# Kernel optimization log

Hardware: AMD Instinct MI355X
Metric: run time of the kernel (lower is better)

Reference implementation:

```python
import jax, jax.numpy as jnp
import numpy as np

B, N, E = 128, 2000, 2000
EMBED, HIDDEN = 256, 512


def setup_inputs() -> dict:
    key = jax.random.key(0)
    k1, k2, k3, k4, k5, k6, k7 = jax.random.split(key, 7)
    node_embeddings = jax.random.normal(k1, (B, N, EMBED), dtype=jnp.float32)
    locs = jax.random.uniform(k2, (B, N, 2), dtype=jnp.float32)
    edge_list = jax.random.randint(k3, (B, E, 2), 0, N, dtype=jnp.int64)
    in_dim = 2 * EMBED + 1
    # Kaiming-ish init for the two Linear layers of edge_scorer
    W1 = jax.random.normal(k4, (in_dim, HIDDEN), dtype=jnp.float32) / np.sqrt(in_dim)
    b1 = jnp.zeros((HIDDEN,), dtype=jnp.float32)
    W2 = jax.random.normal(k5, (HIDDEN, 1), dtype=jnp.float32) / np.sqrt(HIDDEN)
    b2 = jnp.zeros((1,), dtype=jnp.float32)
    return {
        "node_embeddings": node_embeddings,
        "locs": locs,
        "edge_list": edge_list,
        "delete_bias": 0,
        "W1": W1,
        "b1": b1,
        "W2": W2,
        "b2": b2,
    }


def reference(node_embeddings, locs, edge_list, delete_bias, W1, b1, W2, b2):
    # valid mask for -1-padded edges
    valid = (edge_list[..., 0] >= 0) & (edge_list[..., 1] >= 0)  # (B, E)
    edges = jnp.clip(edge_list, 0, None)
    bidx = jnp.arange(node_embeddings.shape[0])[:, None]  # (B, 1)
    i, j = edges[..., 0], edges[..., 1]  # (B, E)
    emb_i = node_embeddings[bidx, i]  # (B, E, D)
    emb_j = node_embeddings[bidx, j]  # (B, E, D)
    d = locs[bidx, i] - locs[bidx, j]  # (B, E, 2)
    dist = jnp.sqrt(jnp.sum(d * d, axis=-1, keepdims=True))  # (B, E, 1)
    feats = jnp.concatenate([emb_i, emb_j, dist], axis=-1)  # (B, E, 2D+1)
    h = jax.nn.relu(jnp.einsum('bef,fh->beh', feats, W1) + b1)
    logits = (jnp.einsum('beh,ho->beo', h, W2) + b2)[..., 0]  # (B, E)
    logits = jnp.where(valid, logits, -jnp.inf)
    return logits + jnp.float32(delete_bias)
```

## Files before the change

kernel.cpp:

```cpp
#include <hip/hip_runtime.h>
#include <math.h>

#define EMBED    256
#define HIDDEN   512
#define Nn       2000
#define Ee       2000
#define BM       128
#define TILES    8
#define NBLK     250
#define NTHREADS 512
#define FP       264

typedef __attribute__((ext_vector_type(8)))  short bf16x8;
typedef __attribute__((ext_vector_type(16))) float f32x16;

static __device__ __forceinline__ short f2bf(float f) {
  unsigned u = __builtin_bit_cast(unsigned, f);
  u += 0x7fffu + ((u >> 16) & 1u);
  return (short)(u >> 16);
}

static __device__ __forceinline__ bf16x8 cvt8(float4 a, float4 b) {
  bf16x8 v;
  v[0]=f2bf(a.x); v[1]=f2bf(a.y); v[2]=f2bf(a.z); v[3]=f2bf(a.w);
  v[4]=f2bf(b.x); v[5]=f2bf(b.y); v[6]=f2bf(b.z); v[7]=f2bf(b.w);
  return v;
}

#define LBAR() do { asm volatile("s_waitcnt lgkmcnt(0)" ::: "memory"); \
                    __builtin_amdgcn_s_barrier(); \
                    asm volatile("" ::: "memory"); } while (0)

__global__ void w1f_kernel(const float* __restrict__ W1, short* __restrict__ W1F) {
  const int t  = blockIdx.x * 512 + threadIdx.x;
  const int l  = t & 63;
  const int tk = (t >> 6) & 31;
  const int tn = t >> 11;
  const int n  = tn * 32 + (l & 31);
  const int k0 = tk * 16 + (l >> 5) * 8;
  bf16x8 v;
#pragma unroll
  for (int q = 0; q < 8; ++q)
    v[q] = f2bf(W1[(size_t)(k0 + q) * HIDDEN + n]);
  *(bf16x8*)(W1F + (size_t)t * 8) = v;
}

__global__ __launch_bounds__(NTHREADS, 2)
void edge_kernel(const float* __restrict__ emb, const float* __restrict__ locs,
                 const int* __restrict__ edges, const int* __restrict__ dbias,
                 const float* __restrict__ W1, const float* __restrict__ b1,
                 const float* __restrict__ W2, const float* __restrict__ b2,
                 const short* __restrict__ W1F, float* __restrict__ out)
{
  __shared__ short feat[2][BM][FP];
  __shared__ float b1_s[HIDDEN], w513_s[HIDDEN], w2_s[HIDDEN];
  __shared__ float part_s[8][BM];
  __shared__ float dist_s[2][BM];
  __shared__ int   valid_s[2][BM];
  __shared__ int   ibase_s[2][BM], jbase_s[2][BM];

  const int tid = threadIdx.x;

  const int orig = blockIdx.x;
  const int xcd  = orig & 7;
  const int idx  = orig >> 3;
  const int sbid = (xcd < 2 ? xcd * 32 : 64 + (xcd - 2) * 31) + idx;
  const int eblk = sbid * (TILES * BM);

  b1_s[tid]   = b1[tid];
  w513_s[tid] = W1[(size_t)512 * HIDDEN + tid];
  w2_s[tid]   = W2[tid];
  const float b2s_base = b2[0] + (float)dbias[0];

  auto do_meta = [&](int T) {
    const int g  = eblk + T * BM + tid;
    const int b  = g / Ee;
    const int i0 = edges[2 * g];
    const int j0 = edges[2 * g + 1];
    valid_s[T & 1][tid] = (i0 >= 0) && (j0 >= 0);
    const int ib = b * Nn + (i0 < 0 ? 0 : i0);
    const int jb = b * Nn + (j0 < 0 ? 0 : j0);
    ibase_s[T & 1][tid] = ib;
    jbase_s[T & 1][tid] = jb;
    const float dx = locs[2 * (size_t)ib]     - locs[2 * (size_t)jb];
    const float dy = locs[2 * (size_t)ib + 1] - locs[2 * (size_t)jb + 1];
    dist_s[T & 1][tid] = sqrtf(dx * dx + dy * dy);
  };

  if (tid < BM) do_meta(0);
  LBAR();

  const int sq = tid & 7;
  const int eh = tid >> 3;
  const int lane = tid & 63;
  const int w    = tid >> 6;
  const int ln31 = lane & 31;
  const int kg   = lane >> 5;

#pragma unroll
  for (int r = 0; r < 2; ++r) {
    const int el = r * 64 + eh;
    const float* src = emb + (size_t)ibase_s[0][el] * EMBED + sq * 8;
#pragma unroll
    for (int m = 0; m < 4; ++m) {
      float4 a  = *(const float4*)(src + m * 64);
      float4 b4 = *(const float4*)(src + m * 64 + 4);
      *(bf16x8*)&feat[0][el][(sq + 8 * m) * 8] = cvt8(a, b4);
    }
  }
  LBAR();

  f32x16 acc[4][2];
#pragma unroll
  for (int et = 0; et < 4; ++et)
#pragma unroll
    for (int nt = 0; nt < 2; ++nt)
#pragma unroll
      for (int q = 0; q < 16; ++q) acc[et][nt][q] = 0.f;

  const short* wfb = W1F + (size_t)(w * 2 * 32) * 512 + lane * 8;

#pragma unroll 1
  for (int p = 0; p < 2 * TILES; ++p) {
    const int bb   = p & 1;
    const int nbuf = bb ^ 1;
    const int half = p & 1;
    const int tps  = (p + 1) >> 1;
    const int sh   = (p + 1) & 1;
    const bool stg = p < 2 * TILES - 1;

    bf16x8 wc0 = *(const bf16x8*)(wfb + (size_t)(half * 16) * 512);
    bf16x8 wc1 = *(const bf16x8*)(wfb + (size_t)(32 + half * 16) * 512);

    float4 hg00, hg01, hg10, hg11;

#pragma unroll
    for (int ks = 0; ks < 16; ++ks) {
      bf16x8 wn0, wn1;
      if (ks < 15) {
        wn0 = *(const bf16x8*)(wfb + (size_t)(half * 16 + ks + 1) * 512);
        wn1 = *(const bf16x8*)(wfb + (size_t)(32 + half * 16 + ks + 1) * 512);
      }

      if (stg && (ks & 3) == 0) {
        const int g2 = ks >> 2;
        const int el = (g2 >> 1) * 64 + eh;
        const int rb = sh ? jbase_s[tps & 1][el] : ibase_s[tps & 1][el];
        const float* src = emb + (size_t)rb * EMBED + sq * 8 + (g2 & 1) * 128;
        hg00 = *(const float4*)(src);
        hg01 = *(const float4*)(src + 4);
        hg10 = *(const float4*)(src + 64);
        hg11 = *(const float4*)(src + 68);
      }
      if (stg && (ks & 3) == 3) {
        const int g2 = ks >> 2;
        const int el = (g2 >> 1) * 64 + eh;
        const int mb = (g2 & 1) * 2;
        *(bf16x8*)&feat[nbuf][el][(sq + 8 * mb) * 8]       = cvt8(hg00, hg01);
        *(bf16x8*)&feat[nbuf][el][(sq + 8 * (mb + 1)) * 8] = cvt8(hg10, hg11);
      }
      if ((p & 1) == 0 && ks == 1 && tid < BM && (p >> 1) + 1 < TILES)
        do_meta((p >> 1) + 1);

#pragma unroll
      for (int et = 0; et < 4; ++et) {
        bf16x8 fb = *(const bf16x8*)(&feat[bb][et * 32 + ln31][ks * 16 + kg * 8]);
        acc[et][0] = __builtin_amdgcn_mfma_f32_32x32x16_bf16(wc0, fb, acc[et][0], 0, 0, 0);
        acc[et][1] = __builtin_amdgcn_mfma_f32_32x32x16_bf16(wc1, fb, acc[et][1], 0, 0, 0);
      }
      wc0 = wn0; wc1 = wn1;
    }
    LBAR();

    if (p & 1) {
      const int t   = p >> 1;
      const int mb2 = t & 1;
      float dv[4], ps[4];
#pragma unroll
      for (int et = 0; et < 4; ++et) {
        dv[et] = dist_s[mb2][et * 32 + ln31];
        ps[et] = 0.f;
      }
#pragma unroll
      for (int nt = 0; nt < 2; ++nt) {
#pragma unroll
        for (int r = 0; r < 16; ++r) {
          const int n = w * 64 + nt * 32 + (r & 3) + ((r >> 2) << 3) + (kg << 2);
          const float bias = b1_s[n];
          const float wd   = w513_s[n];
          const float w2v  = w2_s[n];
#pragma unroll
          for (int et = 0; et < 4; ++et) {
            float pv = acc[et][nt][r] + bias + dv[et] * wd;
            ps[et] += fmaxf(pv, 0.f) * w2v;
          }
        }
      }
#pragma unroll
      for (int et = 0; et < 4; ++et) ps[et] += __shfl_xor(ps[et], 32, 64);
      if (lane < 32) {
#pragma unroll
        for (int et = 0; et < 4; ++et) part_s[w][et * 32 + ln31] = ps[et];
      }
      LBAR();
      if (tid < BM) {
        float s = 0.f;
#pragma unroll
        for (int wv = 0; wv < 8; ++wv) s += part_s[wv][tid];
        float logit = s + b2s_base;
        if (!valid_s[mb2][tid]) logit = -__builtin_inff();
        out[eblk + t * BM + tid] = logit;
      }
#pragma unroll
      for (int et = 0; et < 4; ++et)
#pragma unroll
        for (int nt = 0; nt < 2; ++nt)
#pragma unroll
          for (int q = 0; q < 16; ++q) acc[et][nt][q] = 0.f;
    }
  }
}

extern "C" void kernel_launch(void* const* d_in, const int* in_sizes, int n_in,
                              void* d_out, int out_size, void* d_ws, size_t ws_size,
                              hipStream_t stream) {
  const float* emb   = (const float*)d_in[0];
  const float* locs  = (const float*)d_in[1];
  const int*   edges = (const int*)d_in[2];
  const int*   dbias = (const int*)d_in[3];
  const float* W1    = (const float*)d_in[4];
  const float* b1    = (const float*)d_in[5];
  const float* W2    = (const float*)d_in[6];
  const float* b2    = (const float*)d_in[7];
  float*       out   = (float*)d_out;
  short*       W1F   = (short*)d_ws;

  w1f_kernel<<<dim3(64), dim3(512), 0, stream>>>(W1, W1F);
  edge_kernel<<<dim3(NBLK), dim3(NTHREADS), 0, stream>>>(
      emb, locs, edges, dbias, W1, b1, W2, b2, (const short*)W1F, out);
}
```

Baseline: 151.7 us.

## Split K loop into 64-wide phases with triple-buffered LDS and deeper gather prefetch

Restructures the main loop from 16 half-tile phases of K=256 into 64 phases of K=64. The feature staging buffer becomes three small 72-wide buffers, and each embedding gather is issued two phases before it is consumed. All eight W1 fragments for a phase are loaded up front, and the MFMA cluster runs at raised wave priority with sched_barriers fencing the stages. The intent is to hide global gather latency behind more compute and shrink LDS use. In exchange it adds a block barrier per phase, four times as many as before, and more register pressure from the extra weight and prefetch buffers.

```diff
diff --git a/kernel.cpp b/kernel.cpp
--- a/kernel.cpp
+++ b/kernel.cpp
@@ -9,7 +9,9 @@
 #define TILES    8
 #define NBLK     250
 #define NTHREADS 512
-#define FP       264
+#define PHT      8
+#define NPH      (TILES * PHT)
+#define FP       72
 
 typedef __attribute__((ext_vector_type(8)))  short bf16x8;
 typedef __attribute__((ext_vector_type(16))) float f32x16;
@@ -52,7 +54,7 @@
                  const float* __restrict__ W2, const float* __restrict__ b2,
                  const short* __restrict__ W1F, float* __restrict__ out)
 {
-  __shared__ short feat[2][BM][FP];
+  __shared__ short feat[3][BM][FP];
   __shared__ float b1_s[HIDDEN], w513_s[HIDDEN], w2_s[HIDDEN];
   __shared__ float part_s[8][BM];
   __shared__ float dist_s[2][BM];
@@ -71,6 +73,14 @@
   w513_s[tid] = W1[(size_t)512 * HIDDEN + tid];
   w2_s[tid]   = W2[tid];
   const float b2s_base = b2[0] + (float)dbias[0];
+
+  const int lane = tid & 63;
+  const int w    = tid >> 6;
+  const int ln31 = lane & 31;
+  const int kg   = lane >> 5;
+
+  const int e  = tid >> 2;
+  const int sq = tid & 3;
 
   auto do_meta = [&](int T) {
     const int g  = eblk + T * BM + tid;
@@ -87,98 +97,93 @@
     dist_s[T & 1][tid] = sqrtf(dx * dx + dy * dy);
   };
 
+  auto issue_g = [&](int pp, float4* g) {
+    const int T    = pp >> 3;
+    const int ph   = pp & 7;
+    const int side = ph >> 2;
+    const int q    = ph & 3;
+    const int rb = side ? jbase_s[T & 1][e] : ibase_s[T & 1][e];
+    const float* src = emb + (size_t)rb * EMBED + q * 64 + sq * 16;
+    g[0] = *(const float4*)(src);
+    g[1] = *(const float4*)(src + 4);
+    g[2] = *(const float4*)(src + 8);
+    g[3] = *(const float4*)(src + 12);
+  };
+  auto land_g = [&](int pp, const float4* g) {
+    const int buf = pp % 3;
+    *(bf16x8*)&feat[buf][e][sq * 16]     = cvt8(g[0], g[1]);
+    *(bf16x8*)&feat[buf][e][sq * 16 + 8] = cvt8(g[2], g[3]);
+  };
+
   if (tid < BM) do_meta(0);
   LBAR();
-
-  const int sq = tid & 7;
-  const int eh = tid >> 3;
-  const int lane = tid & 63;
-  const int w    = tid >> 6;
-  const int ln31 = lane & 31;
-  const int kg   = lane >> 5;
-
-#pragma unroll
-  for (int r = 0; r < 2; ++r) {
-    const int el = r * 64 + eh;
-    const float* src = emb + (size_t)ibase_s[0][el] * EMBED + sq * 8;
-#pragma unroll
-    for (int m = 0; m < 4; ++m) {
-      float4 a  = *(const float4*)(src + m * 64);
-      float4 b4 = *(const float4*)(src + m * 64 + 4);
-      *(bf16x8*)&feat[0][el][(sq + 8 * m) * 8] = cvt8(a, b4);
+  float4 ga[4], gb4[4];
+  issue_g(0, ga);
+  issue_g(1, gb4);
+  land_g(0, ga);
+  land_g(1, gb4);
+  issue_g(2, ga);
+  LBAR();
+
+  f32x16 acc[4][2];
+#pragma unroll
+  for (int et = 0; et < 4; ++et)
+#pragma unroll
+    for (int nt = 0; nt < 2; ++nt)
+#pragma unroll
+      for (int q = 0; q < 16; ++q) acc[et][nt][q] = 0.f;
+
+  const short* wfb = W1F + (size_t)(w * 2 * 32) * 512 + lane * 8;
+
+#pragma unroll 1
+  for (int p = 0; p < NPH; ++p) {
+    const int T    = p >> 3;
+    const int ph   = p & 7;
+    const int side = ph >> 2;
+    const int q    = ph & 3;
+    const int buf  = p % 3;
+    const int k16  = side * 16 + q * 4;
+
+    bf16x8 wa[2][4];
+#pragma unroll
+    for (int nt = 0; nt < 2; ++nt)
+#pragma unroll
+      for (int ks = 0; ks < 4; ++ks)
+        wa[nt][ks] = *(const bf16x8*)(wfb + (size_t)(nt * 32 + k16 + ks) * 512);
+    __builtin_amdgcn_sched_barrier(0);
+
+    if (p < NPH - 2) land_g(p + 2, ga);
+    __builtin_amdgcn_sched_barrier(0);
+
+    if (p + 3 < NPH) issue_g(p + 3, ga);
+    __builtin_amdgcn_sched_barrier(0);
+
+#pragma unroll
+    for (int ks = 0; ks < 4; ++ks) {
+      bf16x8 fb0 = *(const bf16x8*)(&feat[buf][ln31][ks * 16 + kg * 8]);
+      bf16x8 fb1 = *(const bf16x8*)(&feat[buf][32 + ln31][ks * 16 + kg * 8]);
+      bf16x8 fb2 = *(const bf16x8*)(&feat[buf][64 + ln31][ks * 16 + kg * 8]);
+      bf16x8 fb3 = *(const bf16x8*)(&feat[buf][96 + ln31][ks * 16 + kg * 8]);
+      __builtin_amdgcn_s_setprio(1);
+      acc[0][0] = __builtin_amdgcn_mfma_f32_32x32x16_bf16(wa[0][ks], fb0, acc[0][0], 0, 0, 0);
+      acc[0][1] = __builtin_amdgcn_mfma_f32_32x32x16_bf16(wa[1][ks], fb0, acc[0][1], 0, 0, 0);
+      acc[1][0] = __builtin_amdgcn_mfma_f32_32x32x16_bf16(wa[0][ks], fb1, acc[1][0], 0, 0, 0);
+      acc[1][1] = __builtin_amdgcn_mfma_f32_32x32x16_bf16(wa[1][ks], fb1, acc[1][1], 0, 0, 0);
+      acc[2][0] = __builtin_amdgcn_mfma_f32_32x32x16_bf16(wa[0][ks], fb2, acc[2][0], 0, 0, 0);
+      acc[2][1] = __builtin_amdgcn_mfma_f32_32x32x16_bf16(wa[1][ks], fb2, acc[2][1], 0, 0, 0);
+      acc[3][0] = __builtin_amdgcn_mfma_f32_32x32x16_bf16(wa[0][ks], fb3, acc[3][0], 0, 0, 0);
+      acc[3][1] = __builtin_amdgcn_mfma_f32_32x32x16_bf16(wa[1][ks], fb3, acc[3][1], 0, 0, 0);
+      __builtin_amdgcn_s_setprio(0);
     }
-  }
-  LBAR();
-
-  f32x16 acc[4][2];
-#pragma unroll
-  for (int et = 0; et < 4; ++et)
-#pragma unroll
-    for (int nt = 0; nt < 2; ++nt)
-#pragma unroll
-      for (int q = 0; q < 16; ++q) acc[et][nt][q] = 0.f;
-
-  const short* wfb = W1F + (size_t)(w * 2 * 32) * 512 + lane * 8;
-
-#pragma unroll 1
-  for (int p = 0; p < 2 * TILES; ++p) {
-    const int bb   = p & 1;
-    const int nbuf = bb ^ 1;
-    const int half = p & 1;
-    const int tps  = (p + 1) >> 1;
-    const int sh   = (p + 1) & 1;
-    const bool stg = p < 2 * TILES - 1;
-
-    bf16x8 wc0 = *(const bf16x8*)(wfb + (size_t)(half * 16) * 512);
-    bf16x8 wc1 = *(const bf16x8*)(wfb + (size_t)(32 + half * 16) * 512);
-
-    float4 hg00, hg01, hg10, hg11;
-
-#pragma unroll
-    for (int ks = 0; ks < 16; ++ks) {
-      bf16x8 wn0, wn1;
-      if (ks < 15) {
-        wn0 = *(const bf16x8*)(wfb + (size_t)(half * 16 + ks + 1) * 512);
-        wn1 = *(const bf16x8*)(wfb + (size_t)(32 + half * 16 + ks + 1) * 512);
-      }
-
-      if (stg && (ks & 3) == 0) {
-        const int g2 = ks >> 2;
-        const int el = (g2 >> 1) * 64 + eh;
-        const int rb = sh ? jbase_s[tps & 1][el] : ibase_s[tps & 1][el];
-        const float* src = emb + (size_t)rb * EMBED + sq * 8 + (g2 & 1) * 128;
-        hg00 = *(const float4*)(src);
-        hg01 = *(const float4*)(src + 4);
-        hg10 = *(const float4*)(src + 64);
-        hg11 = *(const float4*)(src + 68);
-      }
-      if (stg && (ks & 3) == 3) {
-        const int g2 = ks >> 2;
-        const int el = (g2 >> 1) * 64 + eh;
-        const int mb = (g2 & 1) * 2;
-        *(bf16x8*)&feat[nbuf][el][(sq + 8 * mb) * 8]       = cvt8(hg00, hg01);
-        *(bf16x8*)&feat[nbuf][el][(sq + 8 * (mb + 1)) * 8] = cvt8(hg10, hg11);
-      }
-      if ((p & 1) == 0 && ks == 1 && tid < BM && (p >> 1) + 1 < TILES)
-        do_meta((p >> 1) + 1);
-
+
+    if (ph == 2 && T + 1 < TILES && tid < BM) do_meta(T + 1);
+
+    if (ph == 7) {
+      const int par = T & 1;
+      float dv[4], ps[4];
 #pragma unroll
       for (int et = 0; et < 4; ++et) {
-        bf16x8 fb = *(const bf16x8*)(&feat[bb][et * 32 + ln31][ks * 16 + kg * 8]);
-        acc[et][0] = __builtin_amdgcn_mfma_f32_32x32x16_bf16(wc0, fb, acc[et][0], 0, 0, 0);
-        acc[et][1] = __builtin_amdgcn_mfma_f32_32x32x16_bf16(wc1, fb, acc[et][1], 0, 0, 0);
-      }
-      wc0 = wn0; wc1 = wn1;
-    }
-    LBAR();
-
-    if (p & 1) {
-      const int t   = p >> 1;
-      const int mb2 = t & 1;
-      float dv[4], ps[4];
-#pragma unroll
-      for (int et = 0; et < 4; ++et) {
-        dv[et] = dist_s[mb2][et * 32 + ln31];
+        dv[et] = dist_s[par][et * 32 + ln31];
         ps[et] = 0.f;
       }
 #pragma unroll
@@ -208,16 +213,17 @@
 #pragma unroll
         for (int wv = 0; wv < 8; ++wv) s += part_s[wv][tid];
         float logit = s + b2s_base;
-        if (!valid_s[mb2][tid]) logit = -__builtin_inff();
-        out[eblk + t * BM + tid] = logit;
+        if (!valid_s[par][tid]) logit = -__builtin_inff();
+        out[eblk + T * BM + tid] = logit;
       }
 #pragma unroll
       for (int et = 0; et < 4; ++et)
 #pragma unroll
         for (int nt = 0; nt < 2; ++nt)
 #pragma unroll
-          for (int q = 0; q < 16; ++q) acc[et][nt][q] = 0.f;
+          for (int q2 = 0; q2 < 16; ++q2) acc[et][nt][q2] = 0.f;
     }
+    LBAR();
   }
 }
 
```

Result: slower. 468.3 us (+208.6%).
